# Kernel tuning notes

Measured on AMD Instinct MI355X. Metric: run time of the kernel, lower is better.

## Reference

```python
import jax, jax.numpy as jnp
import numpy as np


def setup_inputs() -> dict:
    key = jax.random.key(0)
    ks = jax.random.split(key, 9)
    B, Lq, Lk, D = 8, 2048, 2048, 768
    s = 1.0 / np.sqrt(D)
    return {
        "queries": jax.random.normal(ks[0], (B, Lq, D), dtype=jnp.float32),
        "values": jax.random.normal(ks[1], (B, Lk, D), dtype=jnp.float32),
        "mask": jax.random.randint(ks[2], (B, Lq, Lk), 0, 2) > 0,
        "Wq": jax.random.normal(ks[3], (D, D), dtype=jnp.float32) * s,
        "bq": jax.random.normal(ks[4], (D,), dtype=jnp.float32) * s,
        "Wk": jax.random.normal(ks[5], (D, D), dtype=jnp.float32) * s,
        "bk": jax.random.normal(ks[6], (D,), dtype=jnp.float32) * s,
        "Wv": jax.random.normal(ks[7], (D, D), dtype=jnp.float32) * s,
        "bv": jax.random.normal(ks[8], (D,), dtype=jnp.float32) * s,
    }


def reference(queries, values, mask, Wq, bq, Wk, bk, Wv, bv):
    NEG = jnp.asarray(-1e9, queries.dtype)
    # torch Linear: x @ W.T + b
    q = jnp.einsum("bld,ed->ble", queries, Wq) + bq
    v = jnp.einsum("bld,ed->ble", values, Wv) + bv
    # NOTE (faithful to source): keys are the key-projection of the
    # already value-projected tensor.
    k = jnp.einsum("bld,ed->ble", v, Wk) + bk
    score = jnp.einsum("bqd,bkd->bqk", q, k)  # [B, Lq, Lk]
    score = jnp.where(mask, score, NEG)
    attn = jax.nn.sigmoid(score)  # sigmoid attention, no normalization
    context = jnp.einsum("bqk,bkd->bqd", attn, v)
    return context
```

## Files before the change

### kernel.cpp

```cpp
#include <hip/hip_runtime.h>
#include <hip/hip_bf16.h>

typedef __bf16 bf16_t;
typedef __bf16 bf16x8 __attribute__((ext_vector_type(8)));
typedef __bf16 bf16x4 __attribute__((ext_vector_type(4)));
typedef float  f32x4  __attribute__((ext_vector_type(4)));

#define LDS_DST(p) ((__attribute__((address_space(3))) void*)(p))
#define GLB_SRC(p) ((const __attribute__((address_space(1))) void*)(p))

#define SBAR()   asm volatile("s_barrier" ::: "memory")
#define WLGKM0() asm volatile("s_waitcnt lgkmcnt(0)" ::: "memory")
#define WVM6()   asm volatile("s_waitcnt vmcnt(6)" ::: "memory")
#define WVM0()   asm volatile("s_waitcnt vmcnt(0)" ::: "memory")

__global__ void __launch_bounds__(256)
f32_to_bf16_kernel(const float* __restrict__ in, bf16_t* __restrict__ out, int n4) {
  int i = blockIdx.x * 256 + threadIdx.x;
  if (i < n4) {
    const float4 v = reinterpret_cast<const float4*>(in)[i];
    bf16x4 o;
    o[0] = (bf16_t)v.x; o[1] = (bf16_t)v.y; o[2] = (bf16_t)v.z; o[3] = (bf16_t)v.w;
    reinterpret_cast<bf16x4*>(out)[i] = o;
  }
}

__global__ void __launch_bounds__(256)
transpose_bf16_kernel(const bf16_t* __restrict__ in, bf16_t* __restrict__ out,
                      int R, int C) {
  __shared__ bf16_t tile[64][72];
  const long base = (long)blockIdx.z * R * C;
  const bf16_t* ib = in + base;
  bf16_t* ob = out + base;
  const int r0 = blockIdx.x * 64, c0 = blockIdx.y * 64;
  const int tid = threadIdx.x;
  const int rr = tid >> 3, cg = tid & 7;
#pragma unroll
  for (int p = 0; p < 2; ++p) {
    int row = p * 32 + rr;
    bf16x8 v = *reinterpret_cast<const bf16x8*>(ib + (long)(r0 + row) * C + c0 + cg * 8);
    *reinterpret_cast<bf16x8*>(&tile[row][cg * 8]) = v;
  }
  __syncthreads();
#pragma unroll
  for (int p = 0; p < 2; ++p) {
    int c = p * 32 + rr;
    bf16x8 v;
#pragma unroll
    for (int i = 0; i < 8; ++i) v[i] = tile[cg * 8 + i][c];
    *reinterpret_cast<bf16x8*>(ob + (long)(c0 + c) * R + r0 + cg * 8) = v;
  }
}


__device__ __forceinline__ void stage_A(char* smem, const bf16_t* G, int ldK,
                                        int grow0, int slot, int mh, int kt, int tid) {
  const int wave = tid >> 6, l = tid & 63;
  const int lr = l >> 3;
  const int cgs = ((l & 7) ^ lr) * 8;
#pragma unroll
  for (int j = 0; j < 2; ++j) {
    const int rowbase = j * 128 + mh * 64 + wave * 8;
    __builtin_amdgcn_global_load_lds(
        GLB_SRC(G + (long)(grow0 + rowbase + lr) * ldK + kt + cgs),
        LDS_DST(smem + slot * 65536 + rowbase * 128), 16, 0, 0);
  }
}

__device__ __forceinline__ void stage_B(char* smem, const bf16_t* G, int ldK,
                                        int grow0, int slot, int nh, int kt, int tid) {
  const int wave = tid >> 6, l = tid & 63;
  const int lr = l >> 3;
  const int cgs = ((l & 7) ^ lr) * 8;
#pragma unroll
  for (int j = 0; j < 2; ++j) {
    const int c = wave + j * 8;
    const int rowbase = (c >> 2) * 64 + nh * 32 + (c & 3) * 8;
    __builtin_amdgcn_global_load_lds(
        GLB_SRC(G + (long)(grow0 + rowbase + lr) * ldK + kt + cgs),
        LDS_DST(smem + slot * 65536 + 32768 + rowbase * 128), 16, 0, 0);
  }
}

__device__ __forceinline__ void read_A(const char* smem, int off, bf16x8 (&af)[8], int xk0) {
#pragma unroll
  for (int mf = 0; mf < 4; ++mf)
#pragma unroll
    for (int kk = 0; kk < 2; ++kk)
      af[mf * 2 + kk] = *reinterpret_cast<const bf16x8*>(
          smem + off + mf * 2048 + (kk ? (xk0 ^ 64) : xk0));
}

__device__ __forceinline__ void read_B(const char* smem, int off, bf16x8 (&bf_)[4], int xk0) {
#pragma unroll
  for (int nf = 0; nf < 2; ++nf)
#pragma unroll
    for (int kk = 0; kk < 2; ++kk)
      bf_[nf * 2 + kk] = *reinterpret_cast<const bf16x8*>(
          smem + off + nf * 2048 + (kk ? (xk0 ^ 64) : xk0));
}

template <int MH, int NH>
__device__ __forceinline__ void mfma_q(const bf16x8 (&af)[8], const bf16x8 (&bf_)[4],
                                       f32x4 (&acc)[8][4]) {
#pragma unroll
  for (int mf = 0; mf < 4; ++mf)
#pragma unroll
    for (int nf = 0; nf < 2; ++nf)
#pragma unroll
      for (int kk = 0; kk < 2; ++kk)
        acc[MH * 4 + mf][NH * 2 + nf] = __builtin_amdgcn_mfma_f32_16x16x32_bf16(
            af[mf * 2 + kk], bf_[nf * 2 + kk], acc[MH * 4 + mf][NH * 2 + nf], 0, 0, 0);
}

#define PH_MID() do { SBAR(); WLGKM0(); __builtin_amdgcn_s_setprio(1); } while (0)
#define PH_END() do { __builtin_amdgcn_s_setprio(0); SBAR(); } while (0)
#define PH_END6() do { __builtin_amdgcn_s_setprio(0); WVM6(); SBAR(); } while (0)

template <int MODE>
__global__ void __launch_bounds__(512, 2)
gemm8p_kernel(const bf16_t* __restrict__ A, const bf16_t* __restrict__ B,
              const float* __restrict__ bias, const int* __restrict__ mask,
              void* __restrict__ Cout, int M, int N, int K,
              long sA, long sB, long sC, long sMask) {
  __shared__ __align__(1024) char smem[131072];
  const int bz = blockIdx.z;
  const bf16_t* Ab = A + bz * sA;
  const bf16_t* Bb = B + bz * sB;
  const int bm = blockIdx.x * 256, bn = blockIdx.y * 256;
  const int tid = threadIdx.x;
  const int wave = tid >> 6, lane = tid & 63;
  const int wr = wave >> 2, wc = wave & 3;
  const int l15 = lane & 15, lg = lane >> 4;
  const int xk0 = (lg * 16) ^ ((lane & 7) << 4);
  const int NT = K >> 6;

  const int aoff = wr * 16384 + l15 * 128;
  const int boff = 32768 + wc * 8192 + l15 * 128;

  f32x4 acc[8][4] = {};
  bf16x8 af[8], bf_[4];

  stage_A(smem, Ab, K, bm, 0, 0, 0, tid);
  stage_B(smem, Bb, K, bn, 0, 0, 0, tid);
  stage_B(smem, Bb, K, bn, 0, 1, 0, tid);
  stage_A(smem, Ab, K, bm, 0, 1, 0, tid);
  stage_A(smem, Ab, K, bm, 1, 0, 64, tid);
  stage_B(smem, Bb, K, bn, 1, 1, 64, tid);
  stage_A(smem, Ab, K, bm, 1, 1, 64, tid);
  WVM6();
  SBAR();

  int tp = 0;
  for (; tp + 3 < NT; tp += 2) {
    const int kb = (tp + 1) << 6, kc = (tp + 2) << 6, kd = (tp + 3) << 6;
    read_A(smem, aoff + 0, af, xk0);
    read_B(smem, boff + 0, bf_, xk0);
    stage_B(smem, Bb, K, bn, 1, 0, kb, tid);
    PH_MID(); mfma_q<0, 0>(af, bf_, acc); PH_END();
    read_B(smem, boff + 4096, bf_, xk0);
    stage_A(smem, Ab, K, bm, 0, 0, kc, tid);
    PH_MID(); mfma_q<0, 1>(af, bf_, acc); PH_END();
    read_A(smem, aoff + 8192, af, xk0);
    stage_B(smem, Bb, K, bn, 0, 1, kc, tid);
    PH_MID(); mfma_q<1, 1>(af, bf_, acc); PH_END();
    read_B(smem, boff + 0, bf_, xk0);
    stage_A(smem, Ab, K, bm, 0, 1, kc, tid);
    PH_MID(); mfma_q<1, 0>(af, bf_, acc); PH_END6();
    read_A(smem, aoff + 65536, af, xk0);
    read_B(smem, boff + 65536, bf_, xk0);
    stage_B(smem, Bb, K, bn, 0, 0, kc, tid);
    PH_MID(); mfma_q<0, 0>(af, bf_, acc); PH_END();
    read_B(smem, boff + 65536 + 4096, bf_, xk0);
    stage_A(smem, Ab, K, bm, 1, 0, kd, tid);
    PH_MID(); mfma_q<0, 1>(af, bf_, acc); PH_END();
    read_A(smem, aoff + 65536 + 8192, af, xk0);
    stage_B(smem, Bb, K, bn, 1, 1, kd, tid);
    PH_MID(); mfma_q<1, 1>(af, bf_, acc); PH_END();
    read_B(smem, boff + 65536, bf_, xk0);
    stage_A(smem, Ab, K, bm, 1, 1, kd, tid);
    PH_MID(); mfma_q<1, 0>(af, bf_, acc); PH_END6();
  }

  {
    const int kb = (NT - 1) << 6;
    read_A(smem, aoff + 0, af, xk0);
    read_B(smem, boff + 0, bf_, xk0);
    stage_B(smem, Bb, K, bn, 1, 0, kb, tid);
    PH_MID(); mfma_q<0, 0>(af, bf_, acc); PH_END();
    read_B(smem, boff + 4096, bf_, xk0);
    PH_MID(); mfma_q<0, 1>(af, bf_, acc); PH_END();
    read_A(smem, aoff + 8192, af, xk0);
    PH_MID(); mfma_q<1, 1>(af, bf_, acc); PH_END();
    read_B(smem, boff + 0, bf_, xk0);
    PH_MID(); mfma_q<1, 0>(af, bf_, acc);
    __builtin_amdgcn_s_setprio(0); WVM0(); SBAR();
    read_A(smem, aoff + 65536, af, xk0);
    read_B(smem, boff + 65536, bf_, xk0);
    PH_MID(); mfma_q<0, 0>(af, bf_, acc); PH_END();
    read_B(smem, boff + 65536 + 4096, bf_, xk0);
    PH_MID(); mfma_q<0, 1>(af, bf_, acc); PH_END();
    read_A(smem, aoff + 65536 + 8192, af, xk0);
    PH_MID(); mfma_q<1, 1>(af, bf_, acc); PH_END();
    read_B(smem, boff + 65536, bf_, xk0);
    PH_MID(); mfma_q<1, 0>(af, bf_, acc);
    __builtin_amdgcn_s_setprio(0);
  }

  float* eb = (float*)smem;
  const int lrow = tid >> 3, t7 = tid & 7;
#pragma unroll
  for (int rd = 0; rd < 4; ++rd) {
    __syncthreads();
#pragma unroll
    for (int fi = 0; fi < 2; ++fi)
#pragma unroll
      for (int nf = 0; nf < 4; ++nf)
#pragma unroll
        for (int r = 0; r < 4; ++r) {
          const int lr2 = wr * 32 + fi * 16 + lg * 4 + r;
          eb[lr2 * 256 + wc * 64 + nf * 16 + l15] = acc[rd * 2 + fi][nf][r];
        }
    __syncthreads();
    const int growt = rd * 32 + lrow + ((lrow >> 5) * 96);
    const long rowbase = (long)(bm + growt) * N + bn;
#pragma unroll
    for (int q = 0; q < 8; ++q) {
      const int c4 = (q * 8 + t7) * 4;
      const f32x4 v = *reinterpret_cast<const f32x4*>(&eb[lrow * 256 + c4]);
      if constexpr (MODE == 0) {
        const f32x4 b4 = *reinterpret_cast<const f32x4*>(bias + bn + c4);
        bf16x4 o;
        o[0] = (bf16_t)(v[0] + b4[0]); o[1] = (bf16_t)(v[1] + b4[1]);
        o[2] = (bf16_t)(v[2] + b4[2]); o[3] = (bf16_t)(v[3] + b4[3]);
        *reinterpret_cast<bf16x4*>((bf16_t*)Cout + bz * sC + rowbase + c4) = o;
      } else if constexpr (MODE == 1) {
        const int4 m4 = *reinterpret_cast<const int4*>(mask + bz * sMask + rowbase + c4);
        bf16x4 o;
        o[0] = (bf16_t)(m4.x ? 1.f / (1.f + __expf(-v[0])) : 0.f);
        o[1] = (bf16_t)(m4.y ? 1.f / (1.f + __expf(-v[1])) : 0.f);
        o[2] = (bf16_t)(m4.z ? 1.f / (1.f + __expf(-v[2])) : 0.f);
        o[3] = (bf16_t)(m4.w ? 1.f / (1.f + __expf(-v[3])) : 0.f);
        *reinterpret_cast<bf16x4*>((bf16_t*)Cout + bz * sC + rowbase + c4) = o;
      } else {
        *reinterpret_cast<f32x4*>((float*)Cout + bz * sC + rowbase + c4) = v;
      }
    }
  }
}

extern "C" void kernel_launch(void* const* d_in, const int* in_sizes, int n_in,
                              void* d_out, int out_size, void* d_ws, size_t ws_size,
                              hipStream_t stream) {
  const float* queries = (const float*)d_in[0];
  const float* values  = (const float*)d_in[1];
  const int*   mask    = (const int*)d_in[2];
  const float* Wq = (const float*)d_in[3];
  const float* bq = (const float*)d_in[4];
  const float* Wk = (const float*)d_in[5];
  const float* bk = (const float*)d_in[6];
  const float* Wv = (const float*)d_in[7];
  const float* bv = (const float*)d_in[8];

  char* ws = (char*)d_ws;
  bf16_t* qb  = (bf16_t*)(ws + 0);
  bf16_t* vb  = (bf16_t*)(ws + 25165824);
  bf16_t* wqb = (bf16_t*)(ws + 50331648);
  bf16_t* wkb = (bf16_t*)(ws + 51511296);
  bf16_t* wvb = (bf16_t*)(ws + 52690944);
  bf16_t* qp  = (bf16_t*)(ws + 53870592);
  bf16_t* vp  = (bf16_t*)(ws + 79036416);
  bf16_t* kp  = (bf16_t*)(ws + 104202240);
  bf16_t* vpT = (bf16_t*)(ws + 129368064);
  bf16_t* P   = (bf16_t*)(ws + 154533888);

  const dim3 blk2(512);

  f32_to_bf16_kernel<<<12288, 256, 0, stream>>>(queries, qb, 3145728);
  f32_to_bf16_kernel<<<12288, 256, 0, stream>>>(values, vb, 3145728);
  f32_to_bf16_kernel<<<576, 256, 0, stream>>>(Wq, wqb, 147456);
  f32_to_bf16_kernel<<<576, 256, 0, stream>>>(Wk, wkb, 147456);
  f32_to_bf16_kernel<<<576, 256, 0, stream>>>(Wv, wvb, 147456);

  gemm8p_kernel<0><<<dim3(64, 3, 1), blk2, 0, stream>>>(
      qb, wqb, bq, nullptr, qp, 16384, 768, 768, 0, 0, 0, 0);
  gemm8p_kernel<0><<<dim3(64, 3, 1), blk2, 0, stream>>>(
      vb, wvb, bv, nullptr, vp, 16384, 768, 768, 0, 0, 0, 0);
  gemm8p_kernel<0><<<dim3(64, 3, 1), blk2, 0, stream>>>(
      vp, wkb, bk, nullptr, kp, 16384, 768, 768, 0, 0, 0, 0);

  transpose_bf16_kernel<<<dim3(32, 12, 8), 256, 0, stream>>>(vp, vpT, 2048, 768);

  gemm8p_kernel<1><<<dim3(8, 8, 8), blk2, 0, stream>>>(
      qp, kp, nullptr, mask, P, 2048, 2048, 768,
      (long)2048 * 768, (long)2048 * 768, (long)2048 * 2048, (long)2048 * 2048);

  gemm8p_kernel<2><<<dim3(8, 3, 8), blk2, 0, stream>>>(
      P, vpT, nullptr, nullptr, d_out, 2048, 768, 2048,
      (long)2048 * 2048, (long)768 * 2048, (long)2048 * 768, 0);
}
```

Before: 306.9 us.

## Pack mask to bitfield and drop pre-MFMA barrier and LDS wait in GEMM

A new pre-pass kernel packs the int32 mask into one bit per element with wave ballots. The score GEMM epilogue then reads 32 mask bits per word instead of int4 loads, which shrinks its epilogue memory traffic. Separately, each MFMA phase no longer issues an s_barrier plus an explicit lgkmcnt(0) wait before raising priority, so the per-phase synchronisation is lighter. The price is an extra kernel that still reads the full int mask once. Removing the barrier also risks an LDS race unless compiler-inserted waits and the buffer separation are enough to cover it.

```diff
diff --git a/kernel.cpp b/kernel.cpp
--- a/kernel.cpp
+++ b/kernel.cpp
@@ -10,9 +10,10 @@
 #define GLB_SRC(p) ((const __attribute__((address_space(1))) void*)(p))
 
 #define SBAR()   asm volatile("s_barrier" ::: "memory")
-#define WLGKM0() asm volatile("s_waitcnt lgkmcnt(0)" ::: "memory")
 #define WVM6()   asm volatile("s_waitcnt vmcnt(6)" ::: "memory")
 #define WVM0()   asm volatile("s_waitcnt vmcnt(0)" ::: "memory")
+#define SP1()    __builtin_amdgcn_s_setprio(1)
+#define SP0()    __builtin_amdgcn_s_setprio(0)
 
 __global__ void __launch_bounds__(256)
 f32_to_bf16_kernel(const float* __restrict__ in, bf16_t* __restrict__ out, int n4) {
@@ -22,6 +23,24 @@
     bf16x4 o;
     o[0] = (bf16_t)v.x; o[1] = (bf16_t)v.y; o[2] = (bf16_t)v.z; o[3] = (bf16_t)v.w;
     reinterpret_cast<bf16x4*>(out)[i] = o;
+  }
+}
+
+__global__ void __launch_bounds__(256)
+mask_pack_kernel(const int* __restrict__ mask, unsigned long long* __restrict__ bits) {
+  const long wid = (((long)blockIdx.x * 256 + threadIdx.x) >> 6);
+  const int lane = threadIdx.x & 63;
+  const long base = wid * 512;
+  unsigned long long b[8];
+#pragma unroll
+  for (int i = 0; i < 8; ++i) {
+    const int m = mask[base + i * 64 + lane];
+    b[i] = __ballot(m != 0);
+  }
+  if (lane == 0) {
+    unsigned long long* o = bits + wid * 8;
+#pragma unroll
+    for (int i = 0; i < 8; ++i) o[i] = b[i];
   }
 }
 
@@ -113,14 +132,10 @@
             af[mf * 2 + kk], bf_[nf * 2 + kk], acc[MH * 4 + mf][NH * 2 + nf], 0, 0, 0);
 }
 
-#define PH_MID() do { SBAR(); WLGKM0(); __builtin_amdgcn_s_setprio(1); } while (0)
-#define PH_END() do { __builtin_amdgcn_s_setprio(0); SBAR(); } while (0)
-#define PH_END6() do { __builtin_amdgcn_s_setprio(0); WVM6(); SBAR(); } while (0)
-
 template <int MODE>
 __global__ void __launch_bounds__(512, 2)
 gemm8p_kernel(const bf16_t* __restrict__ A, const bf16_t* __restrict__ B,
-              const float* __restrict__ bias, const int* __restrict__ mask,
+              const float* __restrict__ bias, const unsigned* __restrict__ maskbits,
               void* __restrict__ Cout, int M, int N, int K,
               long sA, long sB, long sC, long sMask) {
   __shared__ __align__(1024) char smem[131072];
@@ -157,29 +172,29 @@
     read_A(smem, aoff + 0, af, xk0);
     read_B(smem, boff + 0, bf_, xk0);
     stage_B(smem, Bb, K, bn, 1, 0, kb, tid);
-    PH_MID(); mfma_q<0, 0>(af, bf_, acc); PH_END();
+    SP1(); mfma_q<0, 0>(af, bf_, acc); SP0(); SBAR();
     read_B(smem, boff + 4096, bf_, xk0);
     stage_A(smem, Ab, K, bm, 0, 0, kc, tid);
-    PH_MID(); mfma_q<0, 1>(af, bf_, acc); PH_END();
+    SP1(); mfma_q<0, 1>(af, bf_, acc); SP0(); SBAR();
     read_A(smem, aoff + 8192, af, xk0);
     stage_B(smem, Bb, K, bn, 0, 1, kc, tid);
-    PH_MID(); mfma_q<1, 1>(af, bf_, acc); PH_END();
+    SP1(); mfma_q<1, 1>(af, bf_, acc); SP0(); SBAR();
     read_B(smem, boff + 0, bf_, xk0);
     stage_A(smem, Ab, K, bm, 0, 1, kc, tid);
-    PH_MID(); mfma_q<1, 0>(af, bf_, acc); PH_END6();
+    SP1(); mfma_q<1, 0>(af, bf_, acc); SP0(); WVM6(); SBAR();
     read_A(smem, aoff + 65536, af, xk0);
     read_B(smem, boff + 65536, bf_, xk0);
     stage_B(smem, Bb, K, bn, 0, 0, kc, tid);
-    PH_MID(); mfma_q<0, 0>(af, bf_, acc); PH_END();
+    SP1(); mfma_q<0, 0>(af, bf_, acc); SP0(); SBAR();
     read_B(smem, boff + 65536 + 4096, bf_, xk0);
     stage_A(smem, Ab, K, bm, 1, 0, kd, tid);
-    PH_MID(); mfma_q<0, 1>(af, bf_, acc); PH_END();
+    SP1(); mfma_q<0, 1>(af, bf_, acc); SP0(); SBAR();
     read_A(smem, aoff + 65536 + 8192, af, xk0);
     stage_B(smem, Bb, K, bn, 1, 1, kd, tid);
-    PH_MID(); mfma_q<1, 1>(af, bf_, acc); PH_END();
+    SP1(); mfma_q<1, 1>(af, bf_, acc); SP0(); SBAR();
     read_B(smem, boff + 65536, bf_, xk0);
     stage_A(smem, Ab, K, bm, 1, 1, kd, tid);
-    PH_MID(); mfma_q<1, 0>(af, bf_, acc); PH_END6();
+    SP1(); mfma_q<1, 0>(af, bf_, acc); SP0(); WVM6(); SBAR();
   }
 
   {
@@ -187,24 +202,22 @@
     read_A(smem, aoff + 0, af, xk0);
     read_B(smem, boff + 0, bf_, xk0);
     stage_B(smem, Bb, K, bn, 1, 0, kb, tid);
-    PH_MID(); mfma_q<0, 0>(af, bf_, acc); PH_END();
+    SP1(); mfma_q<0, 0>(af, bf_, acc); SP0(); SBAR();
     read_B(smem, boff + 4096, bf_, xk0);
-    PH_MID(); mfma_q<0, 1>(af, bf_, acc); PH_END();
+    SP1(); mfma_q<0, 1>(af, bf_, acc); SP0(); SBAR();
     read_A(smem, aoff + 8192, af, xk0);
-    PH_MID(); mfma_q<1, 1>(af, bf_, acc); PH_END();
+    SP1(); mfma_q<1, 1>(af, bf_, acc); SP0(); SBAR();
     read_B(smem, boff + 0, bf_, xk0);
-    PH_MID(); mfma_q<1, 0>(af, bf_, acc);
-    __builtin_amdgcn_s_setprio(0); WVM0(); SBAR();
+    SP1(); mfma_q<1, 0>(af, bf_, acc); SP0(); WVM0(); SBAR();
     read_A(smem, aoff + 65536, af, xk0);
     read_B(smem, boff + 65536, bf_, xk0);
-    PH_MID(); mfma_q<0, 0>(af, bf_, acc); PH_END();
+    SP1(); mfma_q<0, 0>(af, bf_, acc); SP0(); SBAR();
     read_B(smem, boff + 65536 + 4096, bf_, xk0);
-    PH_MID(); mfma_q<0, 1>(af, bf_, acc); PH_END();
+    SP1(); mfma_q<0, 1>(af, bf_, acc); SP0(); SBAR();
     read_A(smem, aoff + 65536 + 8192, af, xk0);
-    PH_MID(); mfma_q<1, 1>(af, bf_, acc); PH_END();
+    SP1(); mfma_q<1, 1>(af, bf_, acc); SP0(); SBAR();
     read_B(smem, boff + 65536, bf_, xk0);
-    PH_MID(); mfma_q<1, 0>(af, bf_, acc);
-    __builtin_amdgcn_s_setprio(0);
+    SP1(); mfma_q<1, 0>(af, bf_, acc); SP0();
   }
 
   float* eb = (float*)smem;
@@ -224,26 +237,38 @@
     __syncthreads();
     const int growt = rd * 32 + lrow + ((lrow >> 5) * 96);
     const long rowbase = (long)(bm + growt) * N + bn;
-#pragma unroll
-    for (int q = 0; q < 8; ++q) {
-      const int c4 = (q * 8 + t7) * 4;
-      const f32x4 v = *reinterpret_cast<const f32x4*>(&eb[lrow * 256 + c4]);
-      if constexpr (MODE == 0) {
-        const f32x4 b4 = *reinterpret_cast<const f32x4*>(bias + bn + c4);
+    if constexpr (MODE == 1) {
+      const unsigned* mw =
+          maskbits + bz * sMask + (long)(bm + growt) * (N >> 5) + (bn >> 5);
+      const uint4 w0 = *reinterpret_cast<const uint4*>(mw);
+      const uint4 w1 = *reinterpret_cast<const uint4*>(mw + 4);
+      const unsigned wq[8] = {w0.x, w0.y, w0.z, w0.w, w1.x, w1.y, w1.z, w1.w};
+#pragma unroll
+      for (int q = 0; q < 8; ++q) {
+        const int c4 = (q * 8 + t7) * 4;
+        const f32x4 v = *reinterpret_cast<const f32x4*>(&eb[lrow * 256 + c4]);
+        const unsigned nib = (wq[q] >> (t7 * 4)) & 0xFu;
         bf16x4 o;
-        o[0] = (bf16_t)(v[0] + b4[0]); o[1] = (bf16_t)(v[1] + b4[1]);
-        o[2] = (bf16_t)(v[2] + b4[2]); o[3] = (bf16_t)(v[3] + b4[3]);
+        o[0] = (bf16_t)((nib & 1u) ? 1.f / (1.f + __expf(-v[0])) : 0.f);
+        o[1] = (bf16_t)((nib & 2u) ? 1.f / (1.f + __expf(-v[1])) : 0.f);
+        o[2] = (bf16_t)((nib & 4u) ? 1.f / (1.f + __expf(-v[2])) : 0.f);
+        o[3] = (bf16_t)((nib & 8u) ? 1.f / (1.f + __expf(-v[3])) : 0.f);
         *reinterpret_cast<bf16x4*>((bf16_t*)Cout + bz * sC + rowbase + c4) = o;
-      } else if constexpr (MODE == 1) {
-        const int4 m4 = *reinterpret_cast<const int4*>(mask + bz * sMask + rowbase + c4);
-        bf16x4 o;
-        o[0] = (bf16_t)(m4.x ? 1.f / (1.f + __expf(-v[0])) : 0.f);
-        o[1] = (bf16_t)(m4.y ? 1.f / (1.f + __expf(-v[1])) : 0.f);
-        o[2] = (bf16_t)(m4.z ? 1.f / (1.f + __expf(-v[2])) : 0.f);
-        o[3] = (bf16_t)(m4.w ? 1.f / (1.f + __expf(-v[3])) : 0.f);
-        *reinterpret_cast<bf16x4*>((bf16_t*)Cout + bz * sC + rowbase + c4) = o;
-      } else {
-        *reinterpret_cast<f32x4*>((float*)Cout + bz * sC + rowbase + c4) = v;
+      }
+    } else {
+#pragma unroll
+      for (int q = 0; q < 8; ++q) {
+        const int c4 = (q * 8 + t7) * 4;
+        const f32x4 v = *reinterpret_cast<const f32x4*>(&eb[lrow * 256 + c4]);
+        if constexpr (MODE == 0) {
+          const f32x4 b4 = *reinterpret_cast<const f32x4*>(bias + bn + c4);
+          bf16x4 o;
+          o[0] = (bf16_t)(v[0] + b4[0]); o[1] = (bf16_t)(v[1] + b4[1]);
+          o[2] = (bf16_t)(v[2] + b4[2]); o[3] = (bf16_t)(v[3] + b4[3]);
+          *reinterpret_cast<bf16x4*>((bf16_t*)Cout + bz * sC + rowbase + c4) = o;
+        } else {
+          *reinterpret_cast<f32x4*>((float*)Cout + bz * sC + rowbase + c4) = v;
+        }
       }
     }
   }
@@ -273,14 +298,17 @@
   bf16_t* kp  = (bf16_t*)(ws + 104202240);
   bf16_t* vpT = (bf16_t*)(ws + 129368064);
   bf16_t* P   = (bf16_t*)(ws + 154533888);
-
-  const dim3 blk2(512);
+  unsigned long long* mbits = (unsigned long long*)(ws + 221642752);
+
+  mask_pack_kernel<<<16384, 256, 0, stream>>>(mask, mbits);
 
   f32_to_bf16_kernel<<<12288, 256, 0, stream>>>(queries, qb, 3145728);
   f32_to_bf16_kernel<<<12288, 256, 0, stream>>>(values, vb, 3145728);
   f32_to_bf16_kernel<<<576, 256, 0, stream>>>(Wq, wqb, 147456);
   f32_to_bf16_kernel<<<576, 256, 0, stream>>>(Wk, wkb, 147456);
   f32_to_bf16_kernel<<<576, 256, 0, stream>>>(Wv, wvb, 147456);
+
+  const dim3 blk2(512);
 
   gemm8p_kernel<0><<<dim3(64, 3, 1), blk2, 0, stream>>>(
       qb, wqb, bq, nullptr, qp, 16384, 768, 768, 0, 0, 0, 0);
@@ -292,8 +320,8 @@
   transpose_bf16_kernel<<<dim3(32, 12, 8), 256, 0, stream>>>(vp, vpT, 2048, 768);
 
   gemm8p_kernel<1><<<dim3(8, 8, 8), blk2, 0, stream>>>(
-      qp, kp, nullptr, mask, P, 2048, 2048, 768,
-      (long)2048 * 768, (long)2048 * 768, (long)2048 * 2048, (long)2048 * 2048);
+      qp, kp, nullptr, (const unsigned*)mbits, P, 2048, 2048, 768,
+      (long)2048 * 768, (long)2048 * 768, (long)2048 * 2048, (long)2048 * 64);
 
   gemm8p_kernel<2><<<dim3(8, 3, 8), blk2, 0, stream>>>(
       P, vpT, nullptr, nullptr, d_out, 2048, 768, 2048,
```

Measured after the change: 303.2 us. Within noise of the previous version (-1.2%).
